# Kernel tuning notes

Hardware: AMD Instinct MI355X
Metric: run time of the kernel (lower is better)

## Reference

```python
import jax, jax.numpy as jnp
import numpy as np

MARGIN = 0.4
ALPHA = 0.01


def _pairwise_dist(emb):
    sq = jnp.sum(emb * emb, axis=1)
    d2 = jnp.maximum(sq[:, None] + sq[None, :] - 2.0 * (emb @ emb.T), 0.0)
    safe = jnp.where(d2 > 0, d2, 1.0)
    return jnp.where(d2 > 0, jnp.sqrt(safe), 0.0)


def setup_inputs() -> dict:
    key = jax.random.key(0)
    ka, kp, kn = jax.random.split(key, 3)
    B, D = 4096, 128
    return {
        "a": jax.random.normal(ka, (B, D), dtype=jnp.float32),
        "p": jax.random.normal(kp, (B, D), dtype=jnp.float32),
        "n": jax.random.normal(kn, (B, D), dtype=jnp.float32),
    }


def reference(a, p, n):
    B = a.shape[0]
    emb = jnp.concatenate([a, p, n], axis=0)            # [3B, D]
    labels = jnp.tile(jnp.arange(B), 3)                 # [3B]
    dist = _pairwise_dist(emb)                          # [3B, 3B]
    same = labels[:, None] == labels[None, :]           # exactly 3 True per row (incl. diag)
    # Every row has >=2 positives (3 incl. self) and >=1 negative, so all rows count.
    pos_max = jnp.max(jnp.where(same, dist, -jnp.inf), axis=1)
    neg_min = jnp.min(jnp.where(same, jnp.inf, dist), axis=1)
    loss = jnp.mean(jnp.maximum(pos_max - neg_min + MARGIN, 0.0))
    reg = jnp.mean((jnp.abs(emb) - 1.0) ** 2)
    return loss + ALPHA * reg
```

## Files before the change

### kernel.cpp

```cpp
#include <hip/hip_runtime.h>

#define NROWS 12288
#define BSZ   4096
#define DIM   128
#define NB    48
#define NTILES (NB * (NB + 1) / 2)
#define COLS_PER_BLOCK 256
#define NSTRIPS (COLS_PER_BLOCK / 32)

typedef __bf16 bf16x8 __attribute__((ext_vector_type(8)));
typedef float  f32x4  __attribute__((ext_vector_type(4)));

__device__ __forceinline__ unsigned short f2bf(float f) {
  unsigned int u = __float_as_uint(f);
  u = u + 0x7FFFu + ((u >> 16) & 1u);
  return (unsigned short)(u >> 16);
}
__device__ __forceinline__ float bf2f(unsigned short h) {
  return __uint_as_float(((unsigned int)h) << 16);
}

__global__ void prep_k(const float* __restrict__ a, const float* __restrict__ p,
                       const float* __restrict__ nn,
                       unsigned short* __restrict__ embh, float* __restrict__ sq,
                       unsigned int* __restrict__ negbits,
                       float* __restrict__ posmax2, float* __restrict__ regpart) {
  const int w = threadIdx.x >> 6, lane = threadIdx.x & 63;
  const int i = blockIdx.x * 4 + w;
  const float2 av = reinterpret_cast<const float2*>(a  + (size_t)i * DIM)[lane];
  const float2 pv = reinterpret_cast<const float2*>(p  + (size_t)i * DIM)[lane];
  const float2 nv = reinterpret_cast<const float2*>(nn + (size_t)i * DIM)[lane];

  const unsigned short ha0 = f2bf(av.x), ha1 = f2bf(av.y);
  const unsigned short hp0 = f2bf(pv.x), hp1 = f2bf(pv.y);
  const unsigned short hn0 = f2bf(nv.x), hn1 = f2bf(nv.y);
  reinterpret_cast<ushort2*>(embh + (size_t)i * DIM)[lane]             = make_ushort2(ha0, ha1);
  reinterpret_cast<ushort2*>(embh + (size_t)(BSZ + i) * DIM)[lane]     = make_ushort2(hp0, hp1);
  reinterpret_cast<ushort2*>(embh + (size_t)(2 * BSZ + i) * DIM)[lane] = make_ushort2(hn0, hn1);

  float rax = bf2f(ha0), ray = bf2f(ha1);
  float rpx = bf2f(hp0), rpy = bf2f(hp1);
  float rnx = bf2f(hn0), rny = bf2f(hn1);
  float sa = rax * rax + ray * ray;
  float sp = rpx * rpx + rpy * rpy;
  float sn = rnx * rnx + rny * rny;

  float t0 = fabsf(av.x) - 1.f, t1 = fabsf(av.y) - 1.f;
  float t2 = fabsf(pv.x) - 1.f, t3 = fabsf(pv.y) - 1.f;
  float t4 = fabsf(nv.x) - 1.f, t5 = fabsf(nv.y) - 1.f;
  float rg = t0 * t0 + t1 * t1 + t2 * t2 + t3 * t3 + t4 * t4 + t5 * t5;

  float dx, dy;
  dx = av.x - pv.x; dy = av.y - pv.y; float dap = dx * dx + dy * dy;
  dx = av.x - nv.x; dy = av.y - nv.y; float dan = dx * dx + dy * dy;
  dx = pv.x - nv.x; dy = pv.y - nv.y; float dpn = dx * dx + dy * dy;

  for (int m = 32; m; m >>= 1) {
    sa  += __shfl_xor(sa, m);  sp  += __shfl_xor(sp, m);  sn  += __shfl_xor(sn, m);
    rg  += __shfl_xor(rg, m);
    dap += __shfl_xor(dap, m); dan += __shfl_xor(dan, m); dpn += __shfl_xor(dpn, m);
  }
  if (lane == 0) {
    sq[i] = sa; sq[BSZ + i] = sp; sq[2 * BSZ + i] = sn;
    negbits[i] = negbits[BSZ + i] = negbits[2 * BSZ + i] = 0x7F800000u;
    posmax2[i]           = fmaxf(dap, dan);
    posmax2[BSZ + i]     = fmaxf(dap, dpn);
    posmax2[2 * BSZ + i] = fmaxf(dan, dpn);
    regpart[i] = rg;
  }
}

__global__ __launch_bounds__(256, 3) void negmin_k(
    const unsigned short* __restrict__ embh,
    const float* __restrict__ sq,
    unsigned int* __restrict__ negbits) {
  __shared__ __align__(16) char ldsB[4][8192];
  __shared__ float cminw[4][COLS_PER_BLOCK];
  const int tid  = threadIdx.x;
  const int w    = tid >> 6;
  const int lane = tid & 63;
  const int c16  = lane & 15;
  const int q    = lane >> 4;

  int rem = blockIdx.x, ti = 0;
  while (rem >= NB - ti) { rem -= NB - ti; ++ti; }
  const int tj   = ti + rem;
  const bool diag = (ti == tj);
  const int wRow    = ti * 256 + w * 64;
  const int colBase = tj * 256;

  bf16x8 afrag[4][4];
  {
    const char* abase = (const char*)embh + (size_t)(wRow + c16) * 256 + q * 16;
#pragma unroll
    for (int mt = 0; mt < 4; ++mt)
#pragma unroll
      for (int ks = 0; ks < 4; ++ks)
        afrag[mt][ks] = *reinterpret_cast<const bf16x8*>(abase + mt * 4096 + ks * 64);
  }

  float sqrow[4][4];
  {
    const int rbase = wRow + q * 4;
#pragma unroll
    for (int mt = 0; mt < 4; ++mt) {
      const f32x4 tv = *reinterpret_cast<const f32x4*>(&sq[rbase + mt * 16]);
#pragma unroll
      for (int r = 0; r < 4; ++r) sqrow[mt][r] = tv[r];
    }
  }

  float minv[4][4];
#pragma unroll
  for (int mt = 0; mt < 4; ++mt)
#pragma unroll
    for (int r = 0; r < 4; ++r) minv[mt][r] = __builtin_inff();

  auto stage = [&](int sidx, int b) {
#pragma unroll
    for (int h = 0; h < 2; ++h) {
      const int kc = w * 2 + h;
      const char* gp = (const char*)embh +
          (size_t)(colBase + sidx * 32 + (kc & 1) * 16 + c16) * 256 +
          (kc >> 1) * 64 + q * 16;
      __builtin_amdgcn_global_load_lds(
          (const __attribute__((address_space(1))) unsigned int*)gp,
          (__attribute__((address_space(3))) unsigned int*)(&ldsB[b][kc * 1024]),
          16, 0, 0);
    }
  };

  auto computeStrip = [&](int sAbs, int slot) {
    const int colStart = colBase + sAbs * 32;
    const float sq0 = sq[colStart + c16];
    const float sq1 = sq[colStart + 16 + c16];

    f32x4 acc[4][2] = {};
#pragma unroll
    for (int ks = 0; ks < 4; ++ks)
#pragma unroll
      for (int ct = 0; ct < 2; ++ct) {
        const bf16x8 bfr =
            *reinterpret_cast<const bf16x8*>(&ldsB[slot][(ks * 2 + ct) * 1024 + lane * 16]);
#pragma unroll
        for (int mt = 0; mt < 4; ++mt)
          acc[mt][ct] =
              __builtin_amdgcn_mfma_f32_16x16x32_bf16(afrag[mt][ks], bfr, acc[mt][ct], 0, 0, 0);
      }

    const int dd = (colStart - wRow) & 4095;
    float cf0 = __builtin_inff(), cf1 = __builtin_inff();
    if (dd < 76 || dd > 4064) {
#pragma unroll
      for (int mt = 0; mt < 4; ++mt)
#pragma unroll
        for (int ct = 0; ct < 2; ++ct) {
          const float sqb = ct ? sq1 : sq0;
          const int lvc = dd + ct * 16 + c16 - q * 4;
#pragma unroll
          for (int r = 0; r < 4; ++r) {
            float e = fmaf(-2.f, acc[mt][ct][r], sqb) + sqrow[mt][r];
            const int K = mt * 16 + r;
            if (lvc == K || lvc == K + 4096) e = __builtin_inff();
            minv[mt][r] = fminf(minv[mt][r], e);
            if (ct) cf1 = fminf(cf1, e); else cf0 = fminf(cf0, e);
          }
        }
    } else {
#pragma unroll
      for (int mt = 0; mt < 4; ++mt)
#pragma unroll
        for (int ct = 0; ct < 2; ++ct) {
          const float sqb = ct ? sq1 : sq0;
#pragma unroll
          for (int r = 0; r < 4; ++r) {
            float e = fmaf(-2.f, acc[mt][ct][r], sqb) + sqrow[mt][r];
            minv[mt][r] = fminf(minv[mt][r], e);
            if (ct) cf1 = fminf(cf1, e); else cf0 = fminf(cf0, e);
          }
        }
    }

    if (!diag) {
      cf0 = fminf(cf0, __shfl_xor(cf0, 16));
      cf0 = fminf(cf0, __shfl_xor(cf0, 32));
      cf1 = fminf(cf1, __shfl_xor(cf1, 16));
      cf1 = fminf(cf1, __shfl_xor(cf1, 32));
      if (q == 0) {
        cminw[w][sAbs * 32 + c16]      = cf0;
        cminw[w][sAbs * 32 + 16 + c16] = cf1;
      }
    }
  };

#pragma unroll
  for (int s = 0; s < 4; ++s) stage(s, s);
  __syncthreads();
#pragma unroll
  for (int s = 0; s < 4; ++s) computeStrip(s, s);

  __syncthreads();
#pragma unroll
  for (int s = 4; s < 8; ++s) stage(s, s - 4);
  __syncthreads();
#pragma unroll
  for (int s = 4; s < 8; ++s) computeStrip(s, s - 4);

#pragma unroll
  for (int mt = 0; mt < 4; ++mt)
#pragma unroll
    for (int r = 0; r < 4; ++r) {
      float v = minv[mt][r];
      v = fminf(v, __shfl_xor(v, 1));
      v = fminf(v, __shfl_xor(v, 2));
      v = fminf(v, __shfl_xor(v, 4));
      v = fminf(v, __shfl_xor(v, 8));
      if (c16 == 0) {
        const int row = wRow + mt * 16 + q * 4 + r;
        atomicMin(&negbits[row], __float_as_uint(fmaxf(v, 0.f)));
      }
    }

  __syncthreads();
  if (!diag) {
    const float m = fminf(fminf(cminw[0][tid], cminw[1][tid]),
                          fminf(cminw[2][tid], cminw[3][tid]));
    atomicMin(&negbits[colBase + tid], __float_as_uint(fmaxf(m, 0.f)));
  }
}

__global__ void final_k(const float* __restrict__ posmax2,
                        const unsigned int* __restrict__ negbits,
                        const float* __restrict__ regpart, float* __restrict__ out) {
  __shared__ float red[16], redr[16];
  const int tid = threadIdx.x;
  float s = 0.f;
  for (int i = tid; i < NROWS; i += 1024) {
    const float pm = sqrtf(posmax2[i]);
    const float nm = sqrtf(__uint_as_float(negbits[i]));
    s += fmaxf(pm - nm + 0.4f, 0.f);
  }
  float rg = 0.f;
  for (int i = tid; i < BSZ; i += 1024) rg += regpart[i];
  for (int m = 32; m; m >>= 1) { s += __shfl_xor(s, m); rg += __shfl_xor(rg, m); }
  if ((tid & 63) == 0) { red[tid >> 6] = s; redr[tid >> 6] = rg; }
  __syncthreads();
  if (tid == 0) {
    float t = 0.f, tr = 0.f;
#pragma unroll
    for (int k = 0; k < 16; ++k) { t += red[k]; tr += redr[k]; }
    out[0] = t / (float)NROWS + 0.01f * (tr / (float)(NROWS * DIM));
  }
}

extern "C" void kernel_launch(void* const* d_in, const int* in_sizes, int n_in,
                              void* d_out, int out_size, void* d_ws, size_t ws_size,
                              hipStream_t stream) {
  const float* a  = (const float*)d_in[0];
  const float* p  = (const float*)d_in[1];
  const float* nn = (const float*)d_in[2];
  float* out = (float*)d_out;
  char* ws = (char*)d_ws;

  const size_t EMBH_BYTES = (size_t)NROWS * DIM * 2;
  unsigned short* embh    = (unsigned short*)ws;
  float*          sq      = (float*)(ws + EMBH_BYTES);
  unsigned int*   negbit  = (unsigned int*)(ws + EMBH_BYTES + (size_t)NROWS * 4);
  float*          pos2    = (float*)(ws + EMBH_BYTES + (size_t)NROWS * 8);
  float*          regpart = (float*)(ws + EMBH_BYTES + (size_t)NROWS * 12);

  prep_k<<<BSZ / 4, 256, 0, stream>>>(a, p, nn, embh, sq, negbit, pos2, regpart);
  negmin_k<<<dim3(NTILES), 256, 0, stream>>>(embh, sq, negbit);
  final_k<<<1, 1024, 0, stream>>>(pos2, negbit, regpart, out);
}
```

Baseline: 119.6 us.

## Load B fragments directly from global instead of staging through LDS

Removes the 32 KB LDS staging buffer and the async global-to-LDS loads with their block barriers. Each wave now loads its B operand fragments straight from global memory into registers inside a non-unrolled strip loop. The goal is to cut LDS usage and synchronisation, which may raise occupancy. In exchange, all four waves load the same column data redundantly through the cache, and there is no prefetch, so load latency is exposed before each strip's MFMAs.

Result: slower. 132.4 us (+10.8%).

```diff
diff --git a/kernel.cpp b/kernel.cpp
--- a/kernel.cpp
+++ b/kernel.cpp
@@ -74,7 +74,6 @@
     const unsigned short* __restrict__ embh,
     const float* __restrict__ sq,
     unsigned int* __restrict__ negbits) {
-  __shared__ __align__(16) char ldsB[4][8192];
   __shared__ float cminw[4][COLS_PER_BLOCK];
   const int tid  = threadIdx.x;
   const int w    = tid >> 6;
@@ -116,37 +115,31 @@
 #pragma unroll
     for (int r = 0; r < 4; ++r) minv[mt][r] = __builtin_inff();
 
-  auto stage = [&](int sidx, int b) {
-#pragma unroll
-    for (int h = 0; h < 2; ++h) {
-      const int kc = w * 2 + h;
-      const char* gp = (const char*)embh +
-          (size_t)(colBase + sidx * 32 + (kc & 1) * 16 + c16) * 256 +
-          (kc >> 1) * 64 + q * 16;
-      __builtin_amdgcn_global_load_lds(
-          (const __attribute__((address_space(1))) unsigned int*)gp,
-          (__attribute__((address_space(3))) unsigned int*)(&ldsB[b][kc * 1024]),
-          16, 0, 0);
-    }
-  };
-
-  auto computeStrip = [&](int sAbs, int slot) {
-    const int colStart = colBase + sAbs * 32;
+  const char* bbase = (const char*)embh + (size_t)(colBase + c16) * 256 + q * 16;
+
+#pragma unroll 1
+  for (int strip = 0; strip < NSTRIPS; ++strip) {
+    const int colStart = colBase + strip * 32;
     const float sq0 = sq[colStart + c16];
     const float sq1 = sq[colStart + 16 + c16];
 
+    bf16x8 bfrag[4][2];
+#pragma unroll
+    for (int ks = 0; ks < 4; ++ks)
+#pragma unroll
+      for (int ct = 0; ct < 2; ++ct)
+        bfrag[ks][ct] = *reinterpret_cast<const bf16x8*>(
+            bbase + (size_t)(strip * 32 + ct * 16) * 256 + ks * 64);
+
     f32x4 acc[4][2] = {};
 #pragma unroll
     for (int ks = 0; ks < 4; ++ks)
 #pragma unroll
-      for (int ct = 0; ct < 2; ++ct) {
-        const bf16x8 bfr =
-            *reinterpret_cast<const bf16x8*>(&ldsB[slot][(ks * 2 + ct) * 1024 + lane * 16]);
+      for (int ct = 0; ct < 2; ++ct)
 #pragma unroll
         for (int mt = 0; mt < 4; ++mt)
-          acc[mt][ct] =
-              __builtin_amdgcn_mfma_f32_16x16x32_bf16(afrag[mt][ks], bfr, acc[mt][ct], 0, 0, 0);
-      }
+          acc[mt][ct] = __builtin_amdgcn_mfma_f32_16x16x32_bf16(
+              afrag[mt][ks], bfrag[ks][ct], acc[mt][ct], 0, 0, 0);
 
     const int dd = (colStart - wRow) & 4095;
     float cf0 = __builtin_inff(), cf1 = __builtin_inff();
@@ -187,24 +180,11 @@
       cf1 = fminf(cf1, __shfl_xor(cf1, 16));
       cf1 = fminf(cf1, __shfl_xor(cf1, 32));
       if (q == 0) {
-        cminw[w][sAbs * 32 + c16]      = cf0;
-        cminw[w][sAbs * 32 + 16 + c16] = cf1;
+        cminw[w][strip * 32 + c16]      = cf0;
+        cminw[w][strip * 32 + 16 + c16] = cf1;
       }
     }
-  };
-
-#pragma unroll
-  for (int s = 0; s < 4; ++s) stage(s, s);
-  __syncthreads();
-#pragma unroll
-  for (int s = 0; s < 4; ++s) computeStrip(s, s);
-
-  __syncthreads();
-#pragma unroll
-  for (int s = 4; s < 8; ++s) stage(s, s - 4);
-  __syncthreads();
-#pragma unroll
-  for (int s = 4; s < 8; ++s) computeStrip(s, s - 4);
+  }
 
 #pragma unroll
   for (int mt = 0; mt < 4; ++mt)
```
